# Kernel optimization log

Measured on AMD Instinct MI355X. Metric: run time of the kernel, lower is better.

## Reference

```python
import jax, jax.numpy as jnp
import numpy as np

EPS_PRE = 1e-05   # constant added to raw scores in the torch module
EPS_NORM = 1e-12  # F.normalize default eps


def setup_inputs() -> dict:
    key = jax.random.key(0)
    kq, kk, kv = jax.random.split(key, 3)
    B, H, S, D = 2, 8, 2048, 64
    query = jax.random.normal(kq, (B, H, S, D), dtype=jnp.float32)
    keys = jax.random.normal(kk, (B, H, S, D), dtype=jnp.float32)
    vals = jax.random.normal(kv, (B, H, S, D), dtype=jnp.float32)
    # causal mask, broadcastable over batch and heads; mask==0 -> score zeroed
    mask = jnp.tril(jnp.ones((S, S), dtype=jnp.int32))[None, None, :, :]
    return {"query": query, "keys": keys, "vals": vals, "mask": mask}


def reference(query, keys, vals, mask):
    # preattn: [B,H,S,S]
    preattn = jnp.einsum("bhsd,bhtd->bhst", query, keys) + EPS_PRE
    preattn = jnp.where(mask == 0, 0.0, preattn)
    # F.normalize(dim=-1): x / max(||x||_2, eps)
    norm = jnp.sqrt(jnp.sum(preattn * preattn, axis=-1, keepdims=True))
    attn = preattn / jnp.maximum(norm, EPS_NORM)
    # dropout is identity in eval mode (reference baseline)
    out = jnp.einsum("bhst,bhtd->bhsd", attn, vals)
    return (out, attn)
```

## Files before the change

kernel.cpp:

```cpp
#include <hip/hip_runtime.h>

#define S_DIM 2048
#define D_DIM 64
#define BH    16
#define EPS_PRE  1e-5f
#define EPS_NORM 1e-12f
#define CT 8

#define WS_G   0
#define WS_M   (BH*32*4096)
#define WS_GV  (2*BH*32*4096)
#define WS_MV  (WS_GV + BH*32*64)
#define WS_RI  (WS_MV + BH*32*64)

typedef __attribute__((ext_vector_type(8))) short bf8;
typedef __attribute__((ext_vector_type(4))) float f32x4;

static __device__ __forceinline__ unsigned fbits(float x){ union{float f;unsigned u;}v; v.f=x; return v.u; }
static __device__ __forceinline__ float bcast(unsigned u){ union{unsigned u;float f;}v; v.u=u; return v.f; }

static __device__ __forceinline__ void split2(float x, unsigned short& h, unsigned short& l){
  unsigned u = fbits(x);
  h = (unsigned short)(u >> 16);
  float lo = x - bcast(u & 0xffff0000u);
  l = (unsigned short)(fbits(lo) >> 16);
}

static __device__ __forceinline__ void pack4f(float x0, float x1, float x2, float x3,
                                              uint2& hh, uint2& ll){
  unsigned u0=fbits(x0),u1=fbits(x1),u2=fbits(x2),u3=fbits(x3);
  hh.x = (u0>>16) | (u1 & 0xffff0000u);
  hh.y = (u2>>16) | (u3 & 0xffff0000u);
  float l0 = x0 - bcast(u0&0xffff0000u);
  float l1 = x1 - bcast(u1&0xffff0000u);
  float l2 = x2 - bcast(u2&0xffff0000u);
  float l3 = x3 - bcast(u3&0xffff0000u);
  ll.x = (fbits(l0)>>16) | (fbits(l1)&0xffff0000u);
  ll.y = (fbits(l2)>>16) | (fbits(l3)&0xffff0000u);
}

static __device__ __forceinline__ f32x4 mfma16(bf8 a, bf8 b, f32x4 c){
  return __builtin_amdgcn_mfma_f32_16x16x32_bf16(a, b, c, 0, 0, 0);
}

static __device__ __forceinline__ void decode(int c, int& rb, int& ck){
  int g = 0;
  while (c >= 4*(g+1)*(g+2)) ++g;
  const int off = c - 4*g*(g+1);
  const int nk = g + 1;
  const int q = off / nk;
  rb = g*8 + q;
  ck = off - q*nk;
}

__global__ __launch_bounds__(256, 4)
void lka_gram(const float* __restrict__ Kg, float* __restrict__ ws,
              float* __restrict__ Og, float* __restrict__ Ag)
{
  __shared__ short tHi[4096], tLo[4096];

  const int tid = threadIdx.x;
  const int wv  = tid >> 6;
  const int ln  = tid & 63;
  const int gq  = ln >> 4;
  const int i16 = ln & 15;

  const int blk = blockIdx.x;
  const int bh  = blk & 15;
  const int ti  = blk >> 4;

  const float* Kb = Kg + (size_t)bh * (S_DIM * D_DIM);

  {
    float4 z = make_float4(0.f,0.f,0.f,0.f);
    float4* p = (float4*)(Og + (size_t)blk * 4096);
    for (int c = tid; c < 1024; c += 256) p[c] = z;
  }
  {
    const int c0 = (ti + 1) * 64;
    const int n4 = (S_DIM - c0) >> 2;
    float* rowp = Ag + (size_t)bh * S_DIM * S_DIM + (size_t)(ti*64 + (tid>>2)) * S_DIM + c0;
    float4 z = make_float4(0.f,0.f,0.f,0.f);
    for (int c = tid & 3; c < n4; c += 4) *(float4*)(rowp + 4*c) = z;
  }

  {
    const int d  = (tid & 31) * 2;
    const int tb = (tid >> 5) * 8;
    float2 rr[8];
    #pragma unroll
    for (int k = 0; k < 8; ++k)
      rr[k] = *(const float2*)(Kb + (size_t)(ti*64 + tb + k) * D_DIM + d);
    #pragma unroll
    for (int dd = 0; dd < 2; ++dd) {
      union { bf8 v; unsigned short h[8]; } H, L;
      #pragma unroll
      for (int k = 0; k < 8; ++k) split2(dd ? rr[k].y : rr[k].x, H.h[k], L.h[k]);
      const int dc = d + dd;
      const int idx = dc*64 + (tb ^ ((dc & 7) << 3));
      *(bf8*)&tHi[idx] = H.v;
      *(bf8*)&tLo[idx] = L.v;
    }
  }

  float gsum = 0.f;
  if (tid < 64) {
    #pragma unroll 8
    for (int t = 0; t < 64; ++t) gsum += Kb[(size_t)(ti*64 + t) * D_DIM + tid];
  }
  __syncthreads();

  const int d2 = wv*16 + i16;
  bf8 bhi[2], blo[2];
  #pragma unroll
  for (int ks = 0; ks < 2; ++ks) {
    const int bi = d2*64 + ((ks*32 + gq*8) ^ ((d2 & 7) << 3));
    bhi[ks] = *(const bf8*)&tHi[bi];
    blo[ks] = *(const bf8*)&tLo[bi];
  }
  f32x4 acc[4];
  #pragma unroll
  for (int rf = 0; rf < 4; ++rf) acc[rf] = (f32x4){0.f,0.f,0.f,0.f};
  #pragma unroll
  for (int ks = 0; ks < 2; ++ks) {
    #pragma unroll
    for (int rf = 0; rf < 4; ++rf) {
      const int d1 = rf*16 + i16;
      const int ai = d1*64 + ((ks*32 + gq*8) ^ ((d1 & 7) << 3));
      bf8 ahi = *(const bf8*)&tHi[ai];
      bf8 alo = *(const bf8*)&tLo[ai];
      acc[rf] = mfma16(ahi, bhi[ks], acc[rf]);
      acc[rf] = mfma16(alo, bhi[ks], acc[rf]);
      acc[rf] = mfma16(ahi, blo[ks], acc[rf]);
    }
  }
  float* Gp = ws + WS_G + (size_t)(bh*32 + ti) * 4096;
  #pragma unroll
  for (int rf = 0; rf < 4; ++rf)
    *(f32x4*)(Gp + d2*64 + rf*16 + gq*4) = acc[rf];

  if (tid < 64) ws[WS_GV + (size_t)(bh*32 + ti)*64 + tid] = gsum;
}

__global__ __launch_bounds__(256, 8)
void lka_prefix(float* __restrict__ ws)
{
  const int tid = threadIdx.x;
  const int blk = blockIdx.x;
  const int bh  = blk >> 2;
  const int r4  = blk & 3;

  const int row = r4*16 + (tid >> 4);
  const int c4  = (tid & 15) * 4;

  const float* Gp = ws + WS_G + (size_t)(bh*32)*4096 + row*64 + c4;
  float*       Mp = ws + WS_M + (size_t)(bh*32)*4096 + row*64 + c4;

  f32x4 acc = (f32x4){0.f,0.f,0.f,0.f};
  #pragma unroll 4
  for (int i = 0; i < 32; ++i) {
    *(f32x4*)(Mp + (size_t)i*4096) = acc;
    f32x4 g = *(const f32x4*)(Gp + (size_t)i*4096);
    acc[0]+=g[0]; acc[1]+=g[1]; acc[2]+=g[2]; acc[3]+=g[3];
  }

  if (r4 == 0 && tid < 64) {
    float a = 0.f;
    #pragma unroll 4
    for (int i = 0; i < 32; ++i) {
      ws[WS_MV + (size_t)(bh*32 + i)*64 + tid] = a;
      a += ws[WS_GV + (size_t)(bh*32 + i)*64 + tid];
    }
  }
}

__global__ __launch_bounds__(256, 4)
void lka_rownorm(const float* __restrict__ Qg, const float* __restrict__ Kg,
                 float* __restrict__ ws)
{
  __shared__ short kHi[4096], kLo[4096];
  __shared__ short mHi[4096], mLo[4096];
  __shared__ float mvS[64];

  const int tid = threadIdx.x;
  const int wv  = tid >> 6;
  const int ln  = tid & 63;
  const int gq  = ln >> 4;
  const int i16 = ln & 15;

  const int blk = blockIdx.x;
  const int bh  = blk & 15;
  const int rb  = blk >> 4;
  const int s0  = rb * 64;

  const float* Qb = Qg + (size_t)bh * (S_DIM * D_DIM);
  const float* Kb = Kg + (size_t)bh * (S_DIM * D_DIM);

  const int srow = s0 + wv*16 + i16;

  {
    const int r  = tid >> 2;
    const int db = (tid & 3) * 16;
    const float* kp = Kb + (size_t)(s0 + r) * D_DIM + db;
    const float* mp = ws + WS_M + (size_t)(bh*32 + rb)*4096 + r*64 + db;
    #pragma unroll
    for (int c = 0; c < 4; ++c) {
      float4 kv = *(const float4*)(kp + 4*c);
      uint2 hh, ll; pack4f(kv.x, kv.y, kv.z, kv.w, hh, ll);
      const int idx = r*64 + ((db + 4*c) ^ ((r & 7) << 3));
      *(uint2*)&kHi[idx] = hh;
      *(uint2*)&kLo[idx] = ll;
      float4 mv = *(const float4*)(mp + 4*c);
      uint2 mh, mlo; pack4f(mv.x, mv.y, mv.z, mv.w, mh, mlo);
      *(uint2*)&mHi[idx] = mh;
      *(uint2*)&mLo[idx] = mlo;
    }
  }
  if (tid < 64) mvS[tid] = ws[WS_MV + (size_t)(bh*32 + rb)*64 + tid];

  bf8 qhi[2], qlo[2];
  #pragma unroll
  for (int ks = 0; ks < 2; ++ks) {
    const float* qp = Qb + (size_t)srow * D_DIM + ks*32 + gq*8;
    float4 a = *(const float4*)qp;
    float4 b = *(const float4*)(qp + 4);
    union { bf8 v; unsigned short h[8]; } H, L;
    float f0[8] = {a.x,a.y,a.z,a.w,b.x,b.y,b.z,b.w};
    #pragma unroll
    for (int j = 0; j < 8; ++j) split2(f0[j], H.h[j], L.h[j]);
    qhi[ks] = H.v; qlo[ks] = L.v;
  }
  __syncthreads();

  f32x4 accS[4], accY[4];
  #pragma unroll
  for (int rf = 0; rf < 4; ++rf) { accS[rf] = (f32x4){0.f,0.f,0.f,0.f}; accY[rf] = (f32x4){0.f,0.f,0.f,0.f}; }
  #pragma unroll
  for (int ks = 0; ks < 2; ++ks) {
    #pragma unroll
    for (int rf = 0; rf < 4; ++rf) {
      const int r   = rf*16 + i16;
      const int idx = r*64 + ((ks*32 + gq*8) ^ ((r & 7) << 3));
      bf8 ahi = *(const bf8*)&kHi[idx];
      bf8 alo = *(const bf8*)&kLo[idx];
      accS[rf] = mfma16(ahi, qhi[ks], accS[rf]);
      accS[rf] = mfma16(alo, qhi[ks], accS[rf]);
      accS[rf] = mfma16(ahi, qlo[ks], accS[rf]);
      bf8 Ahi = *(const bf8*)&mHi[idx];
      bf8 Alo = *(const bf8*)&mLo[idx];
      accY[rf] = mfma16(Ahi, qhi[ks], accY[rf]);
      accY[rf] = mfma16(Alo, qhi[ks], accY[rf]);
      accY[rf] = mfma16(Ahi, qlo[ks], accY[rf]);
    }
  }

  float ssq = 0.f;
  #pragma unroll
  for (int rf = 0; rf < 4; ++rf) {
    f32x4 q4 = *(const f32x4*)(Qb + (size_t)srow * D_DIM + rf*16 + gq*4);
    f32x4 m4 = *(const f32x4*)&mvS[rf*16 + gq*4];
    #pragma unroll
    for (int rg = 0; rg < 4; ++rg) {
      ssq += q4[rg] * (accY[rf][rg] + 2.f*EPS_PRE*m4[rg]);
      const int t = s0 + rf*16 + gq*4 + rg;
      if (t <= srow) { const float x = accS[rf][rg] + EPS_PRE; ssq += x*x; }
    }
  }
  ssq += __shfl_xor(ssq, 16);
  ssq += __shfl_xor(ssq, 32);
  ssq += EPS_PRE*EPS_PRE * (float)(rb*64);
  ssq = fmaxf(ssq, 0.f);
  const float rinv = 1.f / fmaxf(sqrtf(ssq), EPS_NORM);
  if (gq == 0) ws[WS_RI + (size_t)bh*S_DIM + srow] = rinv;
}

__global__ __launch_bounds__(256, 3)
void lka_emit(const float* __restrict__ Qg, const float* __restrict__ Kg,
              const float* __restrict__ Vg, const float* __restrict__ ws,
              float* __restrict__ Og, float* __restrict__ Ag)
{
  __shared__ short kThi[4096], kTlo[4096];
  __shared__ short vThi[4096], vTlo[4096];
  __shared__ short pHi [4096], pLo [4096];

  const int tid = threadIdx.x;
  const int wv  = tid >> 6;
  const int ln  = tid & 63;
  const int gq  = ln >> 4;
  const int i16 = ln & 15;

  const int blk = blockIdx.x;
  const int bh  = blk & 15;
  int rb, ck; decode(blk >> 4, rb, ck);
  const int s0 = rb * 64;

  const float* Qb = Qg + (size_t)bh * (S_DIM * D_DIM);
  const float* Kb = Kg + (size_t)bh * (S_DIM * D_DIM);
  const float* Vb = Vg + (size_t)bh * (S_DIM * D_DIM);
  float* Ob = Og + (size_t)bh * (S_DIM * D_DIM);
  float* Ab = Ag + (size_t)bh * ((size_t)S_DIM * S_DIM);

  const int srow = s0 + wv*16 + i16;

  const float rinv = ws[WS_RI + (size_t)bh*S_DIM + srow];

  bf8 qhi[2], qlo[2];
  #pragma unroll
  for (int ks = 0; ks < 2; ++ks) {
    const float* qp = Qb + (size_t)srow * D_DIM + ks*32 + gq*8;
    float4 a = *(const float4*)qp;
    float4 b = *(const float4*)(qp + 4);
    union { bf8 v; unsigned short h[8]; } H, L;
    float f0[8] = {a.x,a.y,a.z,a.w,b.x,b.y,b.z,b.w};
    #pragma unroll
    for (int j = 0; j < 8; ++j) split2(f0[j], H.h[j], L.h[j]);
    qhi[ks] = H.v; qlo[ks] = L.v;
  }

  auto stageK = [&](int t0){
    const int t  = tid >> 2;
    const int db = (tid & 3) * 16;
    const float* kp = Kb + (size_t)(t0 + t) * D_DIM + db;
    #pragma unroll
    for (int c = 0; c < 4; ++c) {
      float4 kv = *(const float4*)(kp + 4*c);
      uint2 hh, ll; pack4f(kv.x, kv.y, kv.z, kv.w, hh, ll);
      const int idx = t*64 + ((db + 4*c) ^ ((t & 7) << 3));
      *(uint2*)&kThi[idx] = hh;
      *(uint2*)&kTlo[idx] = ll;
    }
  };
  auto stageV = [&](int t0){
    const int d  = (tid & 31) * 2;
    const int tb = (tid >> 5) * 8;
    float2 rr[8];
    #pragma unroll
    for (int k = 0; k < 8; ++k)
      rr[k] = *(const float2*)(Vb + (size_t)(t0 + tb + k) * D_DIM + d);
    #pragma unroll
    for (int dd = 0; dd < 2; ++dd) {
      union { bf8 v; unsigned short h[8]; } H, L;
      #pragma unroll
      for (int k = 0; k < 8; ++k) split2(dd ? rr[k].y : rr[k].x, H.h[k], L.h[k]);
      const int dc = d + dd;
      const int idx = dc*64 + (tb ^ ((dc & 7) << 3));
      *(bf8*)&vThi[idx] = H.v;
      *(bf8*)&vTlo[idx] = L.v;
    }
  };

  f32x4 oacc[4];
  #pragma unroll
  for (int rf = 0; rf < 4; ++rf) oacc[rf] = (f32x4){0.f,0.f,0.f,0.f};

  const int pR = wv*16 + i16;

  const int j0 = ck * CT;
  const int j1 = min(j0 + CT, rb + 1);
  for (int j = j0; j < j1; ++j) {
    __syncthreads();
    stageK(j * 64);
    stageV(j * 64);
    __syncthreads();

    f32x4 acc[4];
    #pragma unroll
    for (int rf = 0; rf < 4; ++rf) acc[rf] = (f32x4){0.f,0.f,0.f,0.f};
    #pragma unroll
    for (int ks = 0; ks < 2; ++ks) {
      #pragma unroll
      for (int rf = 0; rf < 4; ++rf) {
        const int t   = rf*16 + i16;
        const int idx = t*64 + ((ks*32 + gq*8) ^ ((t & 7) << 3));
        bf8 ahi = *(const bf8*)&kThi[idx];
        bf8 alo = *(const bf8*)&kTlo[idx];
        acc[rf] = mfma16(ahi, qhi[ks], acc[rf]);
        acc[rf] = mfma16(alo, qhi[ks], acc[rf]);
        acc[rf] = mfma16(ahi, qlo[ks], acc[rf]);
      }
    }

    #pragma unroll
    for (int rf = 0; rf < 4; ++rf) {
      f32x4 x;
      #pragma unroll
      for (int rg = 0; rg < 4; ++rg) {
        const int t = j*64 + rf*16 + gq*4 + rg;
        float v = acc[rf][rg] + EPS_PRE;
        if (j == rb && t > srow) v = 0.f;
        x[rg] = v * rinv;
      }
      *(f32x4*)(Ab + (size_t)srow * S_DIM + j*64 + rf*16 + gq*4) = x;
      uint2 hh, ll; pack4f(x[0], x[1], x[2], x[3], hh, ll);
      const int pidx = pR*64 + ((rf*16 + gq*4) ^ ((pR & 7) << 3));
      *(uint2*)&pHi[pidx] = hh;
      *(uint2*)&pLo[pidx] = ll;
    }

    #pragma unroll
    for (int ks = 0; ks < 2; ++ks) {
      const int pi = pR*64 + ((ks*32 + gq*8) ^ ((pR & 7) << 3));
      bf8 bhi = *(const bf8*)&pHi[pi];
      bf8 blo = *(const bf8*)&pLo[pi];
      #pragma unroll
      for (int rfd = 0; rfd < 4; ++rfd) {
        const int dct = rfd*16 + i16;
        const int vi  = dct*64 + ((ks*32 + gq*8) ^ ((dct & 7) << 3));
        bf8 ahi = *(const bf8*)&vThi[vi];
        bf8 alo = *(const bf8*)&vTlo[vi];
        oacc[rfd] = mfma16(ahi, bhi, oacc[rfd]);
        oacc[rfd] = mfma16(alo, bhi, oacc[rfd]);
        oacc[rfd] = mfma16(ahi, blo, oacc[rfd]);
      }
    }
  }

  #pragma unroll
  for (int rfd = 0; rfd < 4; ++rfd)
    #pragma unroll
    for (int rg = 0; rg < 4; ++rg)
      atomicAdd(&Ob[(size_t)srow * D_DIM + rfd*16 + gq*4 + rg], oacc[rfd][rg]);
}

extern "C" void kernel_launch(void* const* d_in, const int* in_sizes, int n_in,
                              void* d_out, int out_size, void* d_ws, size_t ws_size,
                              hipStream_t stream) {
  (void)in_sizes; (void)n_in; (void)out_size; (void)ws_size;
  const float* Q = (const float*)d_in[0];
  const float* K = (const float*)d_in[1];
  const float* V = (const float*)d_in[2];
  float* out  = (float*)d_out;
  float* attn = out + (size_t)BH * S_DIM * D_DIM;
  float* ws   = (float*)d_ws;

  lka_gram   <<<dim3(512),  dim3(256), 0, stream>>>(K, ws, out, attn);
  lka_prefix <<<dim3(64),   dim3(256), 0, stream>>>(ws);
  lka_rownorm<<<dim3(512),  dim3(256), 0, stream>>>(Q, K, ws);
  lka_emit   <<<dim3(BH*80),dim3(256), 0, stream>>>(Q, K, V, ws, out, attn);
}
```

Baseline: 445.8 us.

## Prepack K/V into bf16 MFMA fragments once and drop per-tile LDS staging

Adds a pre-pass kernel that converts K and V into hi/lo bf16 split fragments already laid out in MFMA operand order and writes them to workspace. The emit kernel then loads those fragments straight from global memory instead of converting and staging K/V through shared memory for every tile. This removes two barriers per tile and cuts LDS use, which allows a higher occupancy launch bound. The large attention-matrix stores and the zero-fill of the masked region also become nontemporal stores. The cost is an extra kernel launch, extra workspace, and more global traffic for fragments that are re-read by many blocks.

```diff
diff --git a/kernel.cpp b/kernel.cpp
--- a/kernel.cpp
+++ b/kernel.cpp
@@ -12,6 +12,11 @@
 #define WS_GV  (2*BH*32*4096)
 #define WS_MV  (WS_GV + BH*32*64)
 #define WS_RI  (WS_MV + BH*32*64)
+#define FRAG_F (BH*32*2048)
+#define WS_KAH (WS_RI + BH*2048)
+#define WS_KAL (WS_KAH + FRAG_F)
+#define WS_VAH (WS_KAL + FRAG_F)
+#define WS_VAL (WS_VAH + FRAG_F)
 
 typedef __attribute__((ext_vector_type(8))) short bf8;
 typedef __attribute__((ext_vector_type(4))) float f32x4;
@@ -54,6 +59,74 @@
 }
 
 __global__ __launch_bounds__(256, 4)
+void lka_pack(const float* __restrict__ Kg, const float* __restrict__ Vg,
+              float* __restrict__ ws)
+{
+  __shared__ short kHi[4096], kLo[4096];
+  __shared__ short vHi[4096], vLo[4096];
+
+  const int tid = threadIdx.x;
+  const int blk = blockIdx.x;
+  const int bh  = blk & 15;
+  const int ti  = blk >> 4;
+
+  const float* Kb = Kg + (size_t)bh * (S_DIM * D_DIM);
+  const float* Vb = Vg + (size_t)bh * (S_DIM * D_DIM);
+
+  {
+    const int t  = tid >> 2;
+    const int db = (tid & 3) * 16;
+    const float* kp = Kb + (size_t)(ti*64 + t) * D_DIM + db;
+    #pragma unroll
+    for (int c = 0; c < 4; ++c) {
+      float4 kv = *(const float4*)(kp + 4*c);
+      uint2 hh, ll; pack4f(kv.x, kv.y, kv.z, kv.w, hh, ll);
+      const int idx = t*64 + ((db + 4*c) ^ ((t & 7) << 3));
+      *(uint2*)&kHi[idx] = hh;
+      *(uint2*)&kLo[idx] = ll;
+    }
+  }
+  {
+    const int d  = (tid & 31) * 2;
+    const int tb = (tid >> 5) * 8;
+    float2 rr[8];
+    #pragma unroll
+    for (int k = 0; k < 8; ++k)
+      rr[k] = *(const float2*)(Vb + (size_t)(ti*64 + tb + k) * D_DIM + d);
+    #pragma unroll
+    for (int dd = 0; dd < 2; ++dd) {
+      union { bf8 v; unsigned short h[8]; } H, L;
+      #pragma unroll
+      for (int k = 0; k < 8; ++k) split2(dd ? rr[k].y : rr[k].x, H.h[k], L.h[k]);
+      const int dc = d + dd;
+      const int idx = dc*64 + (tb ^ ((dc & 7) << 3));
+      *(bf8*)&vHi[idx] = H.v;
+      *(bf8*)&vLo[idx] = L.v;
+    }
+  }
+  __syncthreads();
+
+  const int w = tid >> 6, ln = tid & 63, gq = ln >> 4, i16 = ln & 15;
+  short* KAh = (short*)(ws + WS_KAH);
+  short* KAl = (short*)(ws + WS_KAL);
+  short* VAh = (short*)(ws + WS_VAH);
+  short* VAl = (short*)(ws + WS_VAL);
+
+  #pragma unroll
+  for (int ff = 0; ff < 2; ++ff) {
+    const int f  = w*2 + ff;
+    const int ks = f >> 2, rf = f & 3;
+    const int r   = rf*16 + i16;
+    const int idx = r*64 + ((ks*32 + gq*8) ^ ((r & 7) << 3));
+    const size_t o = ((size_t)(bh*32 + ti)*8 + f)*512 + ln*8;
+    *(bf8*)(KAh + o) = *(const bf8*)&kHi[idx];
+    *(bf8*)(KAl + o) = *(const bf8*)&kLo[idx];
+    *(bf8*)(VAh + o) = *(const bf8*)&vHi[idx];
+    *(bf8*)(VAl + o) = *(const bf8*)&vLo[idx];
+  }
+}
+
+__global__ __launch_bounds__(256, 4)
 void lka_gram(const float* __restrict__ Kg, float* __restrict__ ws,
               float* __restrict__ Og, float* __restrict__ Ag)
 {
@@ -72,16 +145,17 @@
   const float* Kb = Kg + (size_t)bh * (S_DIM * D_DIM);
 
   {
-    float4 z = make_float4(0.f,0.f,0.f,0.f);
-    float4* p = (float4*)(Og + (size_t)blk * 4096);
+    f32x4 z = (f32x4){0.f,0.f,0.f,0.f};
+    f32x4* p = (f32x4*)(Og + (size_t)blk * 4096);
     for (int c = tid; c < 1024; c += 256) p[c] = z;
   }
   {
     const int c0 = (ti + 1) * 64;
     const int n4 = (S_DIM - c0) >> 2;
     float* rowp = Ag + (size_t)bh * S_DIM * S_DIM + (size_t)(ti*64 + (tid>>2)) * S_DIM + c0;
-    float4 z = make_float4(0.f,0.f,0.f,0.f);
-    for (int c = tid & 3; c < n4; c += 4) *(float4*)(rowp + 4*c) = z;
+    f32x4 z = (f32x4){0.f,0.f,0.f,0.f};
+    for (int c = tid & 3; c < n4; c += 4)
+      __builtin_nontemporal_store(z, (f32x4*)(rowp + 4*c));
   }
 
   {
@@ -274,14 +348,11 @@
   if (gq == 0) ws[WS_RI + (size_t)bh*S_DIM + srow] = rinv;
 }
 
-__global__ __launch_bounds__(256, 3)
-void lka_emit(const float* __restrict__ Qg, const float* __restrict__ Kg,
-              const float* __restrict__ Vg, const float* __restrict__ ws,
+__global__ __launch_bounds__(256, 4)
+void lka_emit(const float* __restrict__ Qg, const float* __restrict__ ws,
               float* __restrict__ Og, float* __restrict__ Ag)
 {
-  __shared__ short kThi[4096], kTlo[4096];
-  __shared__ short vThi[4096], vTlo[4096];
-  __shared__ short pHi [4096], pLo [4096];
+  __shared__ short pHi[4096], pLo[4096];
 
   const int tid = threadIdx.x;
   const int wv  = tid >> 6;
@@ -295,14 +366,17 @@
   const int s0 = rb * 64;
 
   const float* Qb = Qg + (size_t)bh * (S_DIM * D_DIM);
-  const float* Kb = Kg + (size_t)bh * (S_DIM * D_DIM);
-  const float* Vb = Vg + (size_t)bh * (S_DIM * D_DIM);
   float* Ob = Og + (size_t)bh * (S_DIM * D_DIM);
   float* Ab = Ag + (size_t)bh * ((size_t)S_DIM * S_DIM);
 
   const int srow = s0 + wv*16 + i16;
 
   const float rinv = ws[WS_RI + (size_t)bh*S_DIM + srow];
+
+  const short* KAh = (const short*)(ws + WS_KAH);
+  const short* KAl = (const short*)(ws + WS_KAL);
+  const short* VAh = (const short*)(ws + WS_VAH);
+  const short* VAl = (const short*)(ws + WS_VAL);
 
   bf8 qhi[2], qlo[2];
   #pragma unroll
@@ -317,38 +391,6 @@
     qhi[ks] = H.v; qlo[ks] = L.v;
   }
 
-  auto stageK = [&](int t0){
-    const int t  = tid >> 2;
-    const int db = (tid & 3) * 16;
-    const float* kp = Kb + (size_t)(t0 + t) * D_DIM + db;
-    #pragma unroll
-    for (int c = 0; c < 4; ++c) {
-      float4 kv = *(const float4*)(kp + 4*c);
-      uint2 hh, ll; pack4f(kv.x, kv.y, kv.z, kv.w, hh, ll);
-      const int idx = t*64 + ((db + 4*c) ^ ((t & 7) << 3));
-      *(uint2*)&kThi[idx] = hh;
-      *(uint2*)&kTlo[idx] = ll;
-    }
-  };
-  auto stageV = [&](int t0){
-    const int d  = (tid & 31) * 2;
-    const int tb = (tid >> 5) * 8;
-    float2 rr[8];
-    #pragma unroll
-    for (int k = 0; k < 8; ++k)
-      rr[k] = *(const float2*)(Vb + (size_t)(t0 + tb + k) * D_DIM + d);
-    #pragma unroll
-    for (int dd = 0; dd < 2; ++dd) {
-      union { bf8 v; unsigned short h[8]; } H, L;
-      #pragma unroll
-      for (int k = 0; k < 8; ++k) split2(dd ? rr[k].y : rr[k].x, H.h[k], L.h[k]);
-      const int dc = d + dd;
-      const int idx = dc*64 + (tb ^ ((dc & 7) << 3));
-      *(bf8*)&vThi[idx] = H.v;
-      *(bf8*)&vTlo[idx] = L.v;
-    }
-  };
-
   f32x4 oacc[4];
   #pragma unroll
   for (int rf = 0; rf < 4; ++rf) oacc[rf] = (f32x4){0.f,0.f,0.f,0.f};
@@ -358,10 +400,7 @@
   const int j0 = ck * CT;
   const int j1 = min(j0 + CT, rb + 1);
   for (int j = j0; j < j1; ++j) {
-    __syncthreads();
-    stageK(j * 64);
-    stageV(j * 64);
-    __syncthreads();
+    const size_t tb = ((size_t)(bh*32 + j)*8)*512 + ln*8;
 
     f32x4 acc[4];
     #pragma unroll
@@ -370,10 +409,9 @@
     for (int ks = 0; ks < 2; ++ks) {
       #pragma unroll
       for (int rf = 0; rf < 4; ++rf) {
-        const int t   = rf*16 + i16;
-        const int idx = t*64 + ((ks*32 + gq*8) ^ ((t & 7) << 3));
-        bf8 ahi = *(const bf8*)&kThi[idx];
-        bf8 alo = *(const bf8*)&kTlo[idx];
+        const size_t o = tb + (size_t)(ks*4 + rf)*512;
+        bf8 ahi = *(const bf8*)(KAh + o);
+        bf8 alo = *(const bf8*)(KAl + o);
         acc[rf] = mfma16(ahi, qhi[ks], acc[rf]);
         acc[rf] = mfma16(alo, qhi[ks], acc[rf]);
         acc[rf] = mfma16(ahi, qlo[ks], acc[rf]);
@@ -390,7 +428,7 @@
         if (j == rb && t > srow) v = 0.f;
         x[rg] = v * rinv;
       }
-      *(f32x4*)(Ab + (size_t)srow * S_DIM + j*64 + rf*16 + gq*4) = x;
+      __builtin_nontemporal_store(x, (f32x4*)(Ab + (size_t)srow * S_DIM + j*64 + rf*16 + gq*4));
       uint2 hh, ll; pack4f(x[0], x[1], x[2], x[3], hh, ll);
       const int pidx = pR*64 + ((rf*16 + gq*4) ^ ((pR & 7) << 3));
       *(uint2*)&pHi[pidx] = hh;
@@ -404,10 +442,9 @@
       bf8 blo = *(const bf8*)&pLo[pi];
       #pragma unroll
       for (int rfd = 0; rfd < 4; ++rfd) {
-        const int dct = rfd*16 + i16;
-        const int vi  = dct*64 + ((ks*32 + gq*8) ^ ((dct & 7) << 3));
-        bf8 ahi = *(const bf8*)&vThi[vi];
-        bf8 alo = *(const bf8*)&vTlo[vi];
+        const size_t o = tb + (size_t)(ks*4 + rfd)*512;
+        bf8 ahi = *(const bf8*)(VAh + o);
+        bf8 alo = *(const bf8*)(VAl + o);
         oacc[rfd] = mfma16(ahi, bhi, oacc[rfd]);
         oacc[rfd] = mfma16(alo, bhi, oacc[rfd]);
         oacc[rfd] = mfma16(ahi, blo, oacc[rfd]);
@@ -433,8 +470,9 @@
   float* attn = out + (size_t)BH * S_DIM * D_DIM;
   float* ws   = (float*)d_ws;
 
+  lka_pack   <<<dim3(512),  dim3(256), 0, stream>>>(K, V, ws);
   lka_gram   <<<dim3(512),  dim3(256), 0, stream>>>(K, ws, out, attn);
   lka_prefix <<<dim3(64),   dim3(256), 0, stream>>>(ws);
   lka_rownorm<<<dim3(512),  dim3(256), 0, stream>>>(Q, K, ws);
-  lka_emit   <<<dim3(BH*80),dim3(256), 0, stream>>>(Q, K, V, ws, out, attn);
-}
+  lka_emit   <<<dim3(BH*80),dim3(256), 0, stream>>>(Q, ws, out, attn);
+}
```

Result: no change. 437.6 us (-1.9%).
